# Performance work log

Measured on AMD Instinct MI355X. Metric: run time of the kernel, lower is better.

The kernel has to match this reference:

```python
import jax, jax.numpy as jnp
import numpy as np

CUTOFF = 8.0
NUM_G = 50
HID = 128
NUM_INTER = 3
NUM_NODES = 50000
NUM_EDGES = 1600000
NUM_GRAPHS = 128
MAX_Z = 100
LOG2 = float(np.log(2.0))


def ssp(x):
    # PyG ShiftedSoftplus
    return jax.nn.softplus(x) - LOG2


def setup_inputs() -> dict:
    key = jax.random.key(0)
    ks = jax.random.split(key, 20)
    s = 0.1
    pos = jax.random.normal(ks[0], (NUM_NODES, 3), dtype=jnp.float32) * 4.0
    edge_shift = jax.random.normal(ks[1], (NUM_EDGES, 3), dtype=jnp.float32) * 0.5
    z = jax.random.randint(ks[2], (NUM_NODES,), 0, MAX_Z, dtype=jnp.int32)
    edge_index = jax.random.randint(ks[3], (2, NUM_EDGES), 0, NUM_NODES, dtype=jnp.int32)
    batch = jnp.sort(jax.random.randint(ks[4], (NUM_NODES,), 0, NUM_GRAPHS, dtype=jnp.int32))
    emb = jax.random.normal(ks[5], (MAX_Z, HID), dtype=jnp.float32) * s
    mlp_w1 = jax.random.normal(ks[6], (NUM_INTER, NUM_G, HID), dtype=jnp.float32) * s
    mlp_b1 = jnp.zeros((NUM_INTER, HID), jnp.float32)
    mlp_w2 = jax.random.normal(ks[7], (NUM_INTER, HID, HID), dtype=jnp.float32) * s
    mlp_b2 = jnp.zeros((NUM_INTER, HID), jnp.float32)
    cf_w1 = jax.random.normal(ks[8], (NUM_INTER, HID, HID), dtype=jnp.float32) * s  # no bias (PyG lin1)
    cf_w2 = jax.random.normal(ks[9], (NUM_INTER, HID, HID), dtype=jnp.float32) * s
    cf_b2 = jnp.zeros((NUM_INTER, HID), jnp.float32)
    lin_w = jax.random.normal(ks[10], (NUM_INTER, HID, HID), dtype=jnp.float32) * s
    lin_b = jnp.zeros((NUM_INTER, HID), jnp.float32)
    head_w1 = jax.random.normal(ks[11], (HID, HID // 2), dtype=jnp.float32) * s
    head_b1 = jnp.zeros((HID // 2,), jnp.float32)
    head_w2 = jax.random.normal(ks[12], (HID // 2, 1), dtype=jnp.float32) * s
    head_b2 = jnp.zeros((1,), jnp.float32)
    return dict(pos=pos, edge_shift=edge_shift, emb=emb, mlp_w1=mlp_w1, mlp_b1=mlp_b1,
                mlp_w2=mlp_w2, mlp_b2=mlp_b2, cf_w1=cf_w1, cf_w2=cf_w2, cf_b2=cf_b2,
                lin_w=lin_w, lin_b=lin_b, head_w1=head_w1, head_b1=head_b1,
                head_w2=head_w2, head_b2=head_b2, z=z, edge_index=edge_index, batch=batch)


def reference(pos, edge_shift, emb, mlp_w1, mlp_b1, mlp_w2, mlp_b2, cf_w1, cf_w2, cf_b2,
              lin_w, lin_b, head_w1, head_b1, head_w2, head_b2, z, edge_index, batch):
    src, dst = edge_index[0], edge_index[1]
    # edge distances: pos[row] - (pos[col] + shift)
    rel = pos[src] - (pos[dst] + edge_shift)            # [E,3]
    w = jnp.linalg.norm(rel, axis=-1)                   # [E]
    # Gaussian smearing
    offset = jnp.linspace(0.0, CUTOFF, NUM_G, dtype=pos.dtype)
    coeff = -0.5 / (offset[1] - offset[0]) ** 2
    edge_attr = jnp.exp(coeff * (w[:, None] - offset) ** 2)   # [E,50]
    # cosine cutoff
    C = 0.5 * (jnp.cos(w * jnp.pi / CUTOFF) + 1.0)            # [E]
    h = emb[z]                                                # [N,128]
    for i in range(NUM_INTER):
        Wf = (ssp(edge_attr @ mlp_w1[i] + mlp_b1[i]) @ mlp_w2[i] + mlp_b2[i]) * C[:, None]  # [E,128]
        msg = (h @ cf_w1[i])[src] * Wf                   # gather-multiply  [E,128]
        agg = jax.ops.segment_sum(msg, dst, num_segments=NUM_NODES)         # scatter-sum [N,128]
        h = h + (ssp(agg @ cf_w2[i] + cf_b2[i]) @ lin_w[i] + lin_b[i])
    out_atom = ssp(h @ head_w1 + head_b1) @ head_w2 + head_b2               # [N,1]
    sums = jax.ops.segment_sum(out_atom, batch, num_segments=NUM_GRAPHS)    # [G,1]
    counts = jax.ops.segment_sum(jnp.ones((NUM_NODES, 1), out_atom.dtype), batch, num_segments=NUM_GRAPHS)
    return sums / jnp.maximum(counts, 1.0)  # mean readout; out_proj is Identity (128==128)
```

## Files before the change

### kernel.cpp

```cpp
#include <hip/hip_runtime.h>
#include <hip/hip_fp16.h>
#include <math.h>

#define NNODES  50000
#define NEDGES  1600000
#define NGRAPHS 128
#define HID     128
#define NG      50
#define NITER   3
#define TPTS    2048
#define WMAX    12.0f
#define PI_F    3.14159265358979323846f

typedef __attribute__((ext_vector_type(4))) _Float16 half4;
typedef __attribute__((ext_vector_type(4))) float   f32x4;
typedef __attribute__((ext_vector_type(4))) unsigned u32x4;

__device__ __forceinline__ float ssp(float x) {
    float sp = fmaxf(x, 0.0f) + log1pf(expf(-fabsf(x)));
    return sp - 0.69314718055994530942f;
}

__global__ __launch_bounds__(256) void k_init_h(const float* __restrict__ emb,
                                                const int* __restrict__ z,
                                                float* __restrict__ h,
                                                _Float16* __restrict__ hH)
{
    int idx = blockIdx.x * 256 + threadIdx.x;
    int n = idx >> 7, c = idx & 127;
    float v = emb[(z[n] << 7) + c];
    h[idx] = v;
    hH[idx] = (_Float16)v;
}

__global__ __launch_bounds__(128) void k_wt3(const float* __restrict__ w1,
                                             const float* __restrict__ w2,
                                             const float* __restrict__ lw,
                                             _Float16* __restrict__ o1,
                                             _Float16* __restrict__ o2,
                                             _Float16* __restrict__ o3)
{
    int fam = blockIdx.x / 384;
    int rem = blockIdx.x - fam * 384;
    int it = rem >> 7, c = rem & 127, j = threadIdx.x;
    const float* in = (fam == 0) ? w1 : (fam == 1) ? w2 : lw;
    _Float16* out   = (fam == 0) ? o1 : (fam == 1) ? o2 : o3;
    out[(size_t)it * 16384 + c * 128 + j] = (_Float16)in[(size_t)it * 16384 + j * 128 + c];
}

__global__ __launch_bounds__(128) void k_table(const float* __restrict__ W1,
                                               const float* __restrict__ B1,
                                               const float* __restrict__ W2,
                                               const float* __restrict__ B2,
                                               __half* __restrict__ ti)
{
    int it = blockIdx.x / TPTS;
    int pt = blockIdx.x - it * TPTS;
    const float* W1i = W1 + (size_t)it * NG * HID;
    const float* B1i = B1 + (size_t)it * HID;
    const float* W2i = W2 + (size_t)it * HID * HID;
    const float* B2i = B2 + (size_t)it * HID;

    const float step = WMAX / (float)(TPTS - 1);
    float w0 = pt * step;
    int ptn = (pt < TPTS - 1) ? pt + 1 : pt;
    float w1v = ptn * step;

    __shared__ float sEA[2][NG];
    __shared__ float sT1[2][HID];
    int k = threadIdx.x;
    {
        float dx = 8.0f / 49.0f;
        float coeff = -0.5f / (dx * dx);
        if (k < NG) {
            float diff = w0 - (float)k * dx;
            sEA[0][k] = expf(coeff * diff * diff);
        } else if (k >= 64 && k < 64 + NG) {
            float diff = w1v - (float)(k - 64) * dx;
            sEA[1][k - 64] = expf(coeff * diff * diff);
        }
    }
    __syncthreads();
    float a0 = B1i[k], a1 = a0;
    for (int g = 0; g < NG; ++g) {
        float wv = W1i[g * HID + k];
        a0 = fmaf(sEA[0][g], wv, a0);
        a1 = fmaf(sEA[1][g], wv, a1);
    }
    sT1[0][k] = ssp(a0);
    sT1[1][k] = ssp(a1);
    __syncthreads();
    float b0 = B2i[k], b1v = b0;
    for (int j = 0; j < HID; ++j) {
        float wv = W2i[j * HID + k];
        b0  = fmaf(sT1[0][j], wv, b0);
        b1v = fmaf(sT1[1][j], wv, b1v);
    }
    size_t base = ((size_t)it * TPTS + pt) * 256;
    int pair = k >> 1, within = k & 1;
    ti[base + pair * 4 + within]     = __float2half(b0);
    ti[base + pair * 4 + within + 2] = __float2half(b1v - b0);
}

__global__ __launch_bounds__(256) void k_hist(const int* __restrict__ ei,
                                              int* __restrict__ deg)
{
    int e = blockIdx.x * 256 + threadIdx.x;
    if (e >= NEDGES) return;
    atomicAdd(&deg[ei[NEDGES + e]], 1);
}

#define SCAN_T 1024
#define CHUNK  49
__global__ __launch_bounds__(SCAN_T) void k_scan(const int* __restrict__ deg,
                                                 int* __restrict__ rowptr,
                                                 int* __restrict__ cursor)
{
    int tid = threadIdx.x;
    int base = tid * CHUNK;
    int vals[CHUNK];
    int local = 0;
    #pragma unroll
    for (int i = 0; i < CHUNK; ++i) {
        int idx = base + i;
        int v = (idx < NNODES) ? deg[idx] : 0;
        vals[i] = local;
        local += v;
    }
    int lane = tid & 63, wid = tid >> 6;
    int x = local;
    #pragma unroll
    for (int off = 1; off < 64; off <<= 1) {
        int y = __shfl_up(x, off);
        if (lane >= off) x += y;
    }
    __shared__ int wsum[16];
    __shared__ int woff[17];
    if (lane == 63) wsum[wid] = x;
    __syncthreads();
    if (tid == 0) {
        int acc = 0;
        #pragma unroll
        for (int i = 0; i < 16; ++i) { woff[i] = acc; acc += wsum[i]; }
        woff[16] = acc;
    }
    __syncthreads();
    int threadExcl = woff[wid] + x - local;
    #pragma unroll
    for (int i = 0; i < CHUNK; ++i) {
        int idx = base + i;
        if (idx < NNODES) {
            int p = threadExcl + vals[i];
            rowptr[idx] = p;
            cursor[idx] = p;
        }
    }
    if (tid == SCAN_T - 1) rowptr[NNODES] = woff[16];
}

__global__ __launch_bounds__(256) void k_scatter(const int* __restrict__ ei,
                                                 const float* __restrict__ pos,
                                                 const float* __restrict__ shift,
                                                 int* __restrict__ cursor,
                                                 uint2* __restrict__ rec)
{
    int e = blockIdx.x * 256 + threadIdx.x;
    if (e >= NEDGES) return;
    int s = ei[e], d = ei[NEDGES + e];
    float rx = pos[3*s+0] - (pos[3*d+0] + shift[3*e+0]);
    float ry = pos[3*s+1] - (pos[3*d+1] + shift[3*e+1]);
    float rz = pos[3*s+2] - (pos[3*d+2] + shift[3*e+2]);
    float w = sqrtf(rx*rx + ry*ry + rz*rz);
    const float SCALE = (float)(TPTS - 1) / WMAX;
    float t = fminf(w * SCALE, (float)(TPTS - 1));
    int i0 = (int)t; if (i0 > TPTS - 2) i0 = TPTS - 2;
    float fr = t - (float)i0;
    float C = 0.5f * (cosf(w * (PI_F / 8.0f)) + 1.0f);
    __half2 frc = __halves2half2(__float2half(fr), __float2half(C));
    int slot = atomicAdd(&cursor[d], 1);
    rec[slot] = make_uint2((unsigned)s | ((unsigned)i0 << 17), *(unsigned*)&frc);
}

__device__ __forceinline__ void edge_contrib(unsigned rx, unsigned ry, int lane,
                                             const char* __restrict__ hfBase,
                                             const char* __restrict__ tbBase,
                                             float& ax, float& ay)
{
    unsigned sB = (rx & 0x1FFFFu) << 8;
    unsigned tB = (rx >> 17) << 9;
    __half2 frc = *reinterpret_cast<__half2*>(&ry);
    __half2 fr2 = __half2half2(__low2half(frc));
    __half2 c2  = __half2half2(__high2half(frc));
    uint2 tv = *reinterpret_cast<const uint2*>(tbBase + tB + lane * 8);
    unsigned hu = *reinterpret_cast<const unsigned*>(hfBase + sB + lane * 4);
    __half2 hv   = *reinterpret_cast<__half2*>(&hu);
    __half2 vals = *reinterpret_cast<__half2*>(&tv.x);
    __half2 dels = *reinterpret_cast<__half2*>(&tv.y);
    __half2 f2 = __hfma2(fr2, dels, vals);
    __half2 ch = __hmul2(c2, hv);
    ax = fmaf(__low2float(f2),  __low2float(ch),  ax);
    ay = fmaf(__high2float(f2), __high2float(ch), ay);
}

__global__ __launch_bounds__(256) void k_gather(const uint2* __restrict__ rec,
                                                const int* __restrict__ rowptr,
                                                const __half* __restrict__ hfH,
                                                const __half* __restrict__ tableH,
                                                __half2* __restrict__ aggH)
{
    int node = blockIdx.x * 4 + (threadIdx.x >> 6);
    int lane = threadIdx.x & 63;
    const char* hfBase = (const char*)hfH;
    const char* tbBase = (const char*)tableH;
    int beg = rowptr[node], end = rowptr[node + 1];
    float ax0 = 0.f, ay0 = 0.f, ax1 = 0.f, ay1 = 0.f;
    int k = beg;
    if ((k & 1) && k < end) {
        uint2 r = rec[k];
        edge_contrib(r.x, r.y, lane, hfBase, tbBase, ax0, ay0);
        ++k;
    }
    for (; k + 8 <= end; k += 8) {
        u32x4 ra = __builtin_nontemporal_load(reinterpret_cast<const u32x4*>(rec + k));
        u32x4 rb = __builtin_nontemporal_load(reinterpret_cast<const u32x4*>(rec + k + 2));
        u32x4 rc = __builtin_nontemporal_load(reinterpret_cast<const u32x4*>(rec + k + 4));
        u32x4 rd = __builtin_nontemporal_load(reinterpret_cast<const u32x4*>(rec + k + 6));
        edge_contrib(ra.x, ra.y, lane, hfBase, tbBase, ax0, ay0);
        edge_contrib(ra.z, ra.w, lane, hfBase, tbBase, ax1, ay1);
        edge_contrib(rb.x, rb.y, lane, hfBase, tbBase, ax0, ay0);
        edge_contrib(rb.z, rb.w, lane, hfBase, tbBase, ax1, ay1);
        edge_contrib(rc.x, rc.y, lane, hfBase, tbBase, ax0, ay0);
        edge_contrib(rc.z, rc.w, lane, hfBase, tbBase, ax1, ay1);
        edge_contrib(rd.x, rd.y, lane, hfBase, tbBase, ax0, ay0);
        edge_contrib(rd.z, rd.w, lane, hfBase, tbBase, ax1, ay1);
    }
    for (; k + 2 <= end; k += 2) {
        u32x4 ra = __builtin_nontemporal_load(reinterpret_cast<const u32x4*>(rec + k));
        edge_contrib(ra.x, ra.y, lane, hfBase, tbBase, ax0, ay0);
        edge_contrib(ra.z, ra.w, lane, hfBase, tbBase, ax1, ay1);
    }
    if (k < end) {
        uint2 r = rec[k];
        edge_contrib(r.x, r.y, lane, hfBase, tbBase, ax0, ay0);
    }
    aggH[(size_t)node * 64 + lane] = __floats2half2_rn(ax0 + ax1, ay0 + ay1);
}

__global__ __launch_bounds__(256) void k_ngemm_mfma(const _Float16* __restrict__ hH,
                                                    const _Float16* __restrict__ Wt,
                                                    _Float16* __restrict__ outH)
{
    int tid = threadIdx.x;
    int wave = tid >> 6, l = tid & 63;
    int lr = l & 15, lg = l >> 4;
    int r0 = blockIdx.x * 16;
    f32x4 acc[2];
    acc[0] = (f32x4){0.f, 0.f, 0.f, 0.f};
    acc[1] = (f32x4){0.f, 0.f, 0.f, 0.f};
    const _Float16* aRow = hH + (size_t)(r0 + lr) * HID;
    #pragma unroll
    for (int kk = 0; kk < 8; ++kk) {
        half4 a = *(const half4*)(aRow + kk * 16 + lg * 4);
        #pragma unroll
        for (int c = 0; c < 2; ++c) {
            int ct = wave * 2 + c;
            half4 b = *(const half4*)(Wt + (size_t)(ct * 16 + lr) * HID + kk * 16 + lg * 4);
            acc[c] = __builtin_amdgcn_mfma_f32_16x16x16f16(a, b, acc[c], 0, 0, 0);
        }
    }
    #pragma unroll
    for (int c = 0; c < 2; ++c) {
        int col = (wave * 2 + c) * 16 + lr;
        #pragma unroll
        for (int r = 0; r < 4; ++r)
            outH[(size_t)(r0 + lg * 4 + r) * HID + col] = (_Float16)acc[c][r];
    }
}

__global__ __launch_bounds__(256) void k_update_mfma(const _Float16* __restrict__ aggH,
                                                     const _Float16* __restrict__ W2t,
                                                     const float* __restrict__ B2,
                                                     const _Float16* __restrict__ Lt,
                                                     const float* __restrict__ LB,
                                                     float* __restrict__ h,
                                                     _Float16* __restrict__ hH,
                                                     const _Float16* __restrict__ W1n,
                                                     _Float16* __restrict__ hfOut)
{
    __shared__ _Float16 sT[16 * 128];
    int tid = threadIdx.x;
    int wave = tid >> 6, l = tid & 63;
    int lr = l & 15, lg = l >> 4;
    int r0 = blockIdx.x * 16;

    f32x4 acc[2];
    acc[0] = (f32x4){0.f, 0.f, 0.f, 0.f};
    acc[1] = (f32x4){0.f, 0.f, 0.f, 0.f};
    const _Float16* aRow = aggH + (size_t)(r0 + lr) * HID;
    #pragma unroll
    for (int kk = 0; kk < 8; ++kk) {
        half4 a = *(const half4*)(aRow + kk * 16 + lg * 4);
        #pragma unroll
        for (int c = 0; c < 2; ++c) {
            int ct = wave * 2 + c;
            half4 b = *(const half4*)(W2t + (size_t)(ct * 16 + lr) * HID + kk * 16 + lg * 4);
            acc[c] = __builtin_amdgcn_mfma_f32_16x16x16f16(a, b, acc[c], 0, 0, 0);
        }
    }
    #pragma unroll
    for (int c = 0; c < 2; ++c) {
        int col = (wave * 2 + c) * 16 + lr;
        float bias = B2[col];
        #pragma unroll
        for (int r = 0; r < 4; ++r) {
            int rl = lg * 4 + r;
            float v = ssp(acc[c][r] + bias);
            int byte = rl * 256 + col * 2;
            byte ^= (rl & 7) << 4;
            *(_Float16*)((char*)sT + byte) = (_Float16)v;
        }
    }
    __syncthreads();
    f32x4 acc2[2];
    acc2[0] = (f32x4){0.f, 0.f, 0.f, 0.f};
    acc2[1] = (f32x4){0.f, 0.f, 0.f, 0.f};
    #pragma unroll
    for (int kk = 0; kk < 8; ++kk) {
        int byte = lr * 256 + (kk * 16 + lg * 4) * 2;
        byte ^= (lr & 7) << 4;
        half4 a = *(const half4*)((char*)sT + byte);
        #pragma unroll
        for (int c = 0; c < 2; ++c) {
            int ct = wave * 2 + c;
            half4 b = *(const half4*)(Lt + (size_t)(ct * 16 + lr) * HID + kk * 16 + lg * 4);
            acc2[c] = __builtin_amdgcn_mfma_f32_16x16x16f16(a, b, acc2[c], 0, 0, 0);
        }
    }
    __syncthreads();
    _Float16 hnew[2][4];
    #pragma unroll
    for (int c = 0; c < 2; ++c) {
        int col = (wave * 2 + c) * 16 + lr;
        float lb = LB[col];
        #pragma unroll
        for (int r = 0; r < 4; ++r) {
            int row = r0 + lg * 4 + r;
            float hv = h[(size_t)row * HID + col] + acc2[c][r] + lb;
            h[(size_t)row * HID + col] = hv;
            hH[(size_t)row * HID + col] = (_Float16)hv;
            hnew[c][r] = (_Float16)hv;
        }
    }
    if (W1n) {
        #pragma unroll
        for (int c = 0; c < 2; ++c) {
            int col = (wave * 2 + c) * 16 + lr;
            #pragma unroll
            for (int r = 0; r < 4; ++r) {
                int rl = lg * 4 + r;
                int byte = rl * 256 + col * 2;
                byte ^= (rl & 7) << 4;
                *(_Float16*)((char*)sT + byte) = hnew[c][r];
            }
        }
        __syncthreads();
        f32x4 acc3[2];
        acc3[0] = (f32x4){0.f, 0.f, 0.f, 0.f};
        acc3[1] = (f32x4){0.f, 0.f, 0.f, 0.f};
        #pragma unroll
        for (int kk = 0; kk < 8; ++kk) {
            int byte = lr * 256 + (kk * 16 + lg * 4) * 2;
            byte ^= (lr & 7) << 4;
            half4 a = *(const half4*)((char*)sT + byte);
            #pragma unroll
            for (int c = 0; c < 2; ++c) {
                int ct = wave * 2 + c;
                half4 b = *(const half4*)(W1n + (size_t)(ct * 16 + lr) * HID + kk * 16 + lg * 4);
                acc3[c] = __builtin_amdgcn_mfma_f32_16x16x16f16(a, b, acc3[c], 0, 0, 0);
            }
        }
        #pragma unroll
        for (int c = 0; c < 2; ++c) {
            int col = (wave * 2 + c) * 16 + lr;
            #pragma unroll
            for (int r = 0; r < 4; ++r)
                hfOut[(size_t)(r0 + lg * 4 + r) * HID + col] = (_Float16)acc3[c][r];
        }
    }
}

__global__ __launch_bounds__(512) void k_head(const float* __restrict__ h,
                                              const float* __restrict__ w1,
                                              const float* __restrict__ b1,
                                              const float* __restrict__ w2,
                                              const float* __restrict__ b2,
                                              const int* __restrict__ batch,
                                              float* __restrict__ sums_pad)
{
    __shared__ float sA[128 * 132];
    int r0 = blockIdx.x * 128;
    int tid = threadIdx.x;
    for (int idx = tid; idx < 128 * 32; idx += 512) {
        int r = idx >> 5, c4 = idx & 31;
        int row = r0 + r;
        float4 v = make_float4(0.f, 0.f, 0.f, 0.f);
        if (row < NNODES) v = *(const float4*)(h + (size_t)row * HID + c4 * 4);
        *(float4*)(&sA[r * 132 + c4 * 4]) = v;
    }
    __syncthreads();
    int tx = tid & 7, ty = tid >> 3;
    int cc = tx * 8, ee = ty * 2;
    float acc[2][8];
    {
        float4 b0 = *(const float4*)(b1 + cc);
        float4 bb = *(const float4*)(b1 + cc + 4);
        #pragma unroll
        for (int e = 0; e < 2; ++e) {
            acc[e][0]=b0.x; acc[e][1]=b0.y; acc[e][2]=b0.z; acc[e][3]=b0.w;
            acc[e][4]=bb.x; acc[e][5]=bb.y; acc[e][6]=bb.z; acc[e][7]=bb.w;
        }
    }
    #pragma unroll 4
    for (int j = 0; j < HID; ++j) {
        float a0 = sA[(ee + 0) * 132 + j];
        float a1 = sA[(ee + 1) * 132 + j];
        float4 w0 = *(const float4*)(w1 + (size_t)j * 64 + cc);
        float4 wv1 = *(const float4*)(w1 + (size_t)j * 64 + cc + 4);
        float wv[8] = {w0.x,w0.y,w0.z,w0.w,wv1.x,wv1.y,wv1.z,wv1.w};
        #pragma unroll
        for (int c = 0; c < 8; ++c) {
            acc[0][c] = fmaf(a0, wv[c], acc[0][c]);
            acc[1][c] = fmaf(a1, wv[c], acc[1][c]);
        }
    }
    float4 w2a = *(const float4*)(w2 + cc);
    float4 w2b = *(const float4*)(w2 + cc + 4);
    float w2v[8] = {w2a.x,w2a.y,w2a.z,w2a.w,w2b.x,w2b.y,w2b.z,w2b.w};
    float bias2 = b2[0];
    #pragma unroll
    for (int e = 0; e < 2; ++e) {
        float part = 0.f;
        #pragma unroll
        for (int c = 0; c < 8; ++c) part = fmaf(ssp(acc[e][c]), w2v[c], part);
        part += __shfl_down(part, 4, 8);
        part += __shfl_down(part, 2, 8);
        part += __shfl_down(part, 1, 8);
        if (tx == 0) {
            int row = r0 + ee + e;
            if (row < NNODES) {
                int b = batch[row];
                atomicAdd(&sums_pad[b * 16], part + bias2);
            }
        }
    }
}

__global__ void k_final(const float* __restrict__ sums_pad,
                        const int* __restrict__ batch,
                        float* __restrict__ out)
{
    int g = threadIdx.x;
    if (g >= NGRAPHS) return;
    int lo = 0, hi = NNODES;
    while (lo < hi) { int mid = (lo + hi) >> 1; if (batch[mid] < g) lo = mid + 1; else hi = mid; }
    int a = lo;
    lo = 0; hi = NNODES;
    while (lo < hi) { int mid = (lo + hi) >> 1; if (batch[mid] < g + 1) lo = mid + 1; else hi = mid; }
    float cnt = (float)(lo - a);
    out[g] = sums_pad[g * 16] / fmaxf(cnt, 1.0f);
}

extern "C" void kernel_launch(void* const* d_in, const int* in_sizes, int n_in,
                              void* d_out, int out_size, void* d_ws, size_t ws_size,
                              hipStream_t stream)
{
    const float* pos     = (const float*)d_in[0];
    const float* shift   = (const float*)d_in[1];
    const float* emb     = (const float*)d_in[2];
    const float* mlp_w1  = (const float*)d_in[3];
    const float* mlp_b1  = (const float*)d_in[4];
    const float* mlp_w2  = (const float*)d_in[5];
    const float* mlp_b2  = (const float*)d_in[6];
    const float* cf_w1   = (const float*)d_in[7];
    const float* cf_w2   = (const float*)d_in[8];
    const float* cf_b2   = (const float*)d_in[9];
    const float* lin_w   = (const float*)d_in[10];
    const float* lin_b   = (const float*)d_in[11];
    const float* head_w1 = (const float*)d_in[12];
    const float* head_b1 = (const float*)d_in[13];
    const float* head_w2 = (const float*)d_in[14];
    const float* head_b2 = (const float*)d_in[15];
    const int*   z       = (const int*)d_in[16];
    const int*   ei      = (const int*)d_in[17];
    const int*   batch   = (const int*)d_in[18];
    float* out = (float*)d_out;

    float* ws = (float*)d_ws;
    size_t off = 0;
    float*    h       = ws + off; off += (size_t)NNODES * HID;
    _Float16* hH      = (_Float16*)(ws + off); off += (size_t)(NNODES + 64) * HID / 2;
    _Float16* hfH     = (_Float16*)(ws + off); off += (size_t)(NNODES + 64) * HID / 2;
    _Float16* aggH    = (_Float16*)(ws + off); off += (size_t)(NNODES + 64) * HID / 2;
    __half*   tableH  = (__half*)(ws + off); off += (size_t)3 * TPTS * 256 / 2;
    _Float16* w1t     = (_Float16*)(ws + off); off += (size_t)3 * HID * HID / 2;
    _Float16* w2t     = (_Float16*)(ws + off); off += (size_t)3 * HID * HID / 2;
    _Float16* lwt     = (_Float16*)(ws + off); off += (size_t)3 * HID * HID / 2;
    uint2*    rec     = (uint2*)(ws + off); off += (size_t)2 * NEDGES;
    int*      rowptr  = (int*)(ws + off); off += NNODES + 1;
    int*      deg     = (int*)(ws + off); off += NNODES;
    int*      cursor  = (int*)(ws + off); off += NNODES;
    float*    sums_pad= ws + off; off += NGRAPHS * 16;

    hipMemsetAsync(deg, 0, NNODES * sizeof(int), stream);
    hipMemsetAsync(sums_pad, 0, NGRAPHS * 16 * sizeof(float), stream);

    k_hist<<<(NEDGES + 255) / 256, 256, 0, stream>>>(ei, deg);
    k_scan<<<1, SCAN_T, 0, stream>>>(deg, rowptr, cursor);
    k_scatter<<<(NEDGES + 255) / 256, 256, 0, stream>>>(ei, pos, shift, cursor, rec);

    k_init_h<<<NNODES * HID / 256, 256, 0, stream>>>(emb, z, h, hH);
    k_table<<<3 * TPTS, 128, 0, stream>>>(mlp_w1, mlp_b1, mlp_w2, mlp_b2, tableH);
    k_wt3<<<3 * 384, 128, 0, stream>>>(cf_w1, cf_w2, lin_w, w1t, w2t, lwt);

    int gblk = NNODES / 16;
    k_ngemm_mfma<<<gblk, 256, 0, stream>>>(hH, w1t, hfH);
    for (int i = 0; i < NITER; ++i) {
        k_gather<<<NNODES / 4, 256, 0, stream>>>(rec, rowptr, (const __half*)hfH,
                                                 tableH + (size_t)i * TPTS * 256,
                                                 (__half2*)aggH);
        k_update_mfma<<<gblk, 256, 0, stream>>>(aggH, w2t + (size_t)i * HID * HID,
                                                cf_b2 + (size_t)i * HID,
                                                lwt + (size_t)i * HID * HID,
                                                lin_b + (size_t)i * HID, h, hH,
                                                (i < NITER - 1) ? w1t + (size_t)(i + 1) * HID * HID : nullptr,
                                                hfH);
    }
    k_head<<<(NNODES + 127) / 128, 512, 0, stream>>>(h, head_w1, head_b1, head_w2, head_b2, batch, sums_pad);
    k_final<<<1, 128, 0, stream>>>(sums_pad, batch, out);
}
```

Baseline: 1.018 ms.

## Fuse edge gather with node update MLP into one per-iteration kernel

The separate gather kernel and update kernel are merged into one kernel per interaction. Each block gathers 16 nodes' aggregated messages into shared memory and then runs the update GEMMs directly from LDS. This removes the global write and read of the aggregation buffer and one launch per iteration. The filtered features now ping-pong between two buffers so the next iteration's features can be written while other blocks still read the current ones. The cost is that each wave now walks four nodes' edge lists in sequence, and the shared-memory GEMM phase waits on the slowest node, which may reduce memory-level parallelism in the gather.

```diff
diff --git a/kernel.cpp b/kernel.cpp
--- a/kernel.cpp
+++ b/kernel.cpp
@@ -202,50 +202,6 @@
     ay = fmaf(__high2float(f2), __high2float(ch), ay);
 }
 
-__global__ __launch_bounds__(256) void k_gather(const uint2* __restrict__ rec,
-                                                const int* __restrict__ rowptr,
-                                                const __half* __restrict__ hfH,
-                                                const __half* __restrict__ tableH,
-                                                __half2* __restrict__ aggH)
-{
-    int node = blockIdx.x * 4 + (threadIdx.x >> 6);
-    int lane = threadIdx.x & 63;
-    const char* hfBase = (const char*)hfH;
-    const char* tbBase = (const char*)tableH;
-    int beg = rowptr[node], end = rowptr[node + 1];
-    float ax0 = 0.f, ay0 = 0.f, ax1 = 0.f, ay1 = 0.f;
-    int k = beg;
-    if ((k & 1) && k < end) {
-        uint2 r = rec[k];
-        edge_contrib(r.x, r.y, lane, hfBase, tbBase, ax0, ay0);
-        ++k;
-    }
-    for (; k + 8 <= end; k += 8) {
-        u32x4 ra = __builtin_nontemporal_load(reinterpret_cast<const u32x4*>(rec + k));
-        u32x4 rb = __builtin_nontemporal_load(reinterpret_cast<const u32x4*>(rec + k + 2));
-        u32x4 rc = __builtin_nontemporal_load(reinterpret_cast<const u32x4*>(rec + k + 4));
-        u32x4 rd = __builtin_nontemporal_load(reinterpret_cast<const u32x4*>(rec + k + 6));
-        edge_contrib(ra.x, ra.y, lane, hfBase, tbBase, ax0, ay0);
-        edge_contrib(ra.z, ra.w, lane, hfBase, tbBase, ax1, ay1);
-        edge_contrib(rb.x, rb.y, lane, hfBase, tbBase, ax0, ay0);
-        edge_contrib(rb.z, rb.w, lane, hfBase, tbBase, ax1, ay1);
-        edge_contrib(rc.x, rc.y, lane, hfBase, tbBase, ax0, ay0);
-        edge_contrib(rc.z, rc.w, lane, hfBase, tbBase, ax1, ay1);
-        edge_contrib(rd.x, rd.y, lane, hfBase, tbBase, ax0, ay0);
-        edge_contrib(rd.z, rd.w, lane, hfBase, tbBase, ax1, ay1);
-    }
-    for (; k + 2 <= end; k += 2) {
-        u32x4 ra = __builtin_nontemporal_load(reinterpret_cast<const u32x4*>(rec + k));
-        edge_contrib(ra.x, ra.y, lane, hfBase, tbBase, ax0, ay0);
-        edge_contrib(ra.z, ra.w, lane, hfBase, tbBase, ax1, ay1);
-    }
-    if (k < end) {
-        uint2 r = rec[k];
-        edge_contrib(r.x, r.y, lane, hfBase, tbBase, ax0, ay0);
-    }
-    aggH[(size_t)node * 64 + lane] = __floats2half2_rn(ax0 + ax1, ay0 + ay1);
-}
-
 __global__ __launch_bounds__(256) void k_ngemm_mfma(const _Float16* __restrict__ hH,
                                                     const _Float16* __restrict__ Wt,
                                                     _Float16* __restrict__ outH)
@@ -277,29 +233,78 @@
     }
 }
 
-__global__ __launch_bounds__(256) void k_update_mfma(const _Float16* __restrict__ aggH,
-                                                     const _Float16* __restrict__ W2t,
-                                                     const float* __restrict__ B2,
-                                                     const _Float16* __restrict__ Lt,
-                                                     const float* __restrict__ LB,
-                                                     float* __restrict__ h,
-                                                     _Float16* __restrict__ hH,
-                                                     const _Float16* __restrict__ W1n,
-                                                     _Float16* __restrict__ hfOut)
-{
+__global__ __launch_bounds__(256) void k_iter(const uint2* __restrict__ rec,
+                                              const int* __restrict__ rowptr,
+                                              const __half* __restrict__ hfIn,
+                                              const __half* __restrict__ tableH,
+                                              const _Float16* __restrict__ W2t,
+                                              const float* __restrict__ B2,
+                                              const _Float16* __restrict__ Lt,
+                                              const float* __restrict__ LB,
+                                              float* __restrict__ h,
+                                              _Float16* __restrict__ hH,
+                                              const _Float16* __restrict__ W1n,
+                                              _Float16* __restrict__ hfOut)
+{
+    __shared__ _Float16 sAgg[16 * 128];
     __shared__ _Float16 sT[16 * 128];
     int tid = threadIdx.x;
     int wave = tid >> 6, l = tid & 63;
+    int r0 = blockIdx.x * 16;
+    const char* hfBase = (const char*)hfIn;
+    const char* tbBase = (const char*)tableH;
+
+    #pragma unroll
+    for (int j = 0; j < 4; ++j) {
+        int rl = wave * 4 + j;
+        int node = r0 + rl;
+        int beg = rowptr[node], end = rowptr[node + 1];
+        float ax0 = 0.f, ay0 = 0.f, ax1 = 0.f, ay1 = 0.f;
+        int k = beg;
+        if ((k & 1) && k < end) {
+            uint2 r = rec[k];
+            edge_contrib(r.x, r.y, l, hfBase, tbBase, ax0, ay0);
+            ++k;
+        }
+        for (; k + 8 <= end; k += 8) {
+            u32x4 ra = __builtin_nontemporal_load(reinterpret_cast<const u32x4*>(rec + k));
+            u32x4 rb = __builtin_nontemporal_load(reinterpret_cast<const u32x4*>(rec + k + 2));
+            u32x4 rc = __builtin_nontemporal_load(reinterpret_cast<const u32x4*>(rec + k + 4));
+            u32x4 rd = __builtin_nontemporal_load(reinterpret_cast<const u32x4*>(rec + k + 6));
+            edge_contrib(ra.x, ra.y, l, hfBase, tbBase, ax0, ay0);
+            edge_contrib(ra.z, ra.w, l, hfBase, tbBase, ax1, ay1);
+            edge_contrib(rb.x, rb.y, l, hfBase, tbBase, ax0, ay0);
+            edge_contrib(rb.z, rb.w, l, hfBase, tbBase, ax1, ay1);
+            edge_contrib(rc.x, rc.y, l, hfBase, tbBase, ax0, ay0);
+            edge_contrib(rc.z, rc.w, l, hfBase, tbBase, ax1, ay1);
+            edge_contrib(rd.x, rd.y, l, hfBase, tbBase, ax0, ay0);
+            edge_contrib(rd.z, rd.w, l, hfBase, tbBase, ax1, ay1);
+        }
+        for (; k + 2 <= end; k += 2) {
+            u32x4 ra = __builtin_nontemporal_load(reinterpret_cast<const u32x4*>(rec + k));
+            edge_contrib(ra.x, ra.y, l, hfBase, tbBase, ax0, ay0);
+            edge_contrib(ra.z, ra.w, l, hfBase, tbBase, ax1, ay1);
+        }
+        if (k < end) {
+            uint2 r = rec[k];
+            edge_contrib(r.x, r.y, l, hfBase, tbBase, ax0, ay0);
+        }
+        __half2 res = __floats2half2_rn(ax0 + ax1, ay0 + ay1);
+        int byte = rl * 256 + l * 4;
+        byte ^= (rl & 7) << 4;
+        *(__half2*)((char*)sAgg + byte) = res;
+    }
+    __syncthreads();
+
     int lr = l & 15, lg = l >> 4;
-    int r0 = blockIdx.x * 16;
-
     f32x4 acc[2];
     acc[0] = (f32x4){0.f, 0.f, 0.f, 0.f};
     acc[1] = (f32x4){0.f, 0.f, 0.f, 0.f};
-    const _Float16* aRow = aggH + (size_t)(r0 + lr) * HID;
     #pragma unroll
     for (int kk = 0; kk < 8; ++kk) {
-        half4 a = *(const half4*)(aRow + kk * 16 + lg * 4);
+        int byte = lr * 256 + (kk * 16 + lg * 4) * 2;
+        byte ^= (lr & 7) << 4;
+        half4 a = *(const half4*)((char*)sAgg + byte);
         #pragma unroll
         for (int c = 0; c < 2; ++c) {
             int ct = wave * 2 + c;
@@ -321,6 +326,7 @@
         }
     }
     __syncthreads();
+
     f32x4 acc2[2];
     acc2[0] = (f32x4){0.f, 0.f, 0.f, 0.f};
     acc2[1] = (f32x4){0.f, 0.f, 0.f, 0.f};
@@ -336,8 +342,6 @@
             acc2[c] = __builtin_amdgcn_mfma_f32_16x16x16f16(a, b, acc2[c], 0, 0, 0);
         }
     }
-    __syncthreads();
-    _Float16 hnew[2][4];
     #pragma unroll
     for (int c = 0; c < 2; ++c) {
         int col = (wave * 2 + c) * 16 + lr;
@@ -348,21 +352,15 @@
             float hv = h[(size_t)row * HID + col] + acc2[c][r] + lb;
             h[(size_t)row * HID + col] = hv;
             hH[(size_t)row * HID + col] = (_Float16)hv;
-            hnew[c][r] = (_Float16)hv;
-        }
-    }
-    if (W1n) {
-        #pragma unroll
-        for (int c = 0; c < 2; ++c) {
-            int col = (wave * 2 + c) * 16 + lr;
-            #pragma unroll
-            for (int r = 0; r < 4; ++r) {
+            if (W1n) {
                 int rl = lg * 4 + r;
                 int byte = rl * 256 + col * 2;
                 byte ^= (rl & 7) << 4;
-                *(_Float16*)((char*)sT + byte) = hnew[c][r];
+                *(_Float16*)((char*)sAgg + byte) = (_Float16)hv;
             }
         }
+    }
+    if (W1n) {
         __syncthreads();
         f32x4 acc3[2];
         acc3[0] = (f32x4){0.f, 0.f, 0.f, 0.f};
@@ -371,7 +369,7 @@
         for (int kk = 0; kk < 8; ++kk) {
             int byte = lr * 256 + (kk * 16 + lg * 4) * 2;
             byte ^= (lr & 7) << 4;
-            half4 a = *(const half4*)((char*)sT + byte);
+            half4 a = *(const half4*)((char*)sAgg + byte);
             #pragma unroll
             for (int c = 0; c < 2; ++c) {
                 int ct = wave * 2 + c;
@@ -499,8 +497,8 @@
     size_t off = 0;
     float*    h       = ws + off; off += (size_t)NNODES * HID;
     _Float16* hH      = (_Float16*)(ws + off); off += (size_t)(NNODES + 64) * HID / 2;
-    _Float16* hfH     = (_Float16*)(ws + off); off += (size_t)(NNODES + 64) * HID / 2;
-    _Float16* aggH    = (_Float16*)(ws + off); off += (size_t)(NNODES + 64) * HID / 2;
+    _Float16* hfA     = (_Float16*)(ws + off); off += (size_t)(NNODES + 64) * HID / 2;
+    _Float16* hfB     = (_Float16*)(ws + off); off += (size_t)(NNODES + 64) * HID / 2;
     __half*   tableH  = (__half*)(ws + off); off += (size_t)3 * TPTS * 256 / 2;
     _Float16* w1t     = (_Float16*)(ws + off); off += (size_t)3 * HID * HID / 2;
     _Float16* w2t     = (_Float16*)(ws + off); off += (size_t)3 * HID * HID / 2;
@@ -523,17 +521,18 @@
     k_wt3<<<3 * 384, 128, 0, stream>>>(cf_w1, cf_w2, lin_w, w1t, w2t, lwt);
 
     int gblk = NNODES / 16;
-    k_ngemm_mfma<<<gblk, 256, 0, stream>>>(hH, w1t, hfH);
+    k_ngemm_mfma<<<gblk, 256, 0, stream>>>(hH, w1t, hfA);
+    _Float16* hfPing[2] = {hfA, hfB};
     for (int i = 0; i < NITER; ++i) {
-        k_gather<<<NNODES / 4, 256, 0, stream>>>(rec, rowptr, (const __half*)hfH,
-                                                 tableH + (size_t)i * TPTS * 256,
-                                                 (__half2*)aggH);
-        k_update_mfma<<<gblk, 256, 0, stream>>>(aggH, w2t + (size_t)i * HID * HID,
-                                                cf_b2 + (size_t)i * HID,
-                                                lwt + (size_t)i * HID * HID,
-                                                lin_b + (size_t)i * HID, h, hH,
-                                                (i < NITER - 1) ? w1t + (size_t)(i + 1) * HID * HID : nullptr,
-                                                hfH);
+        k_iter<<<gblk, 256, 0, stream>>>(rec, rowptr,
+                                         (const __half*)hfPing[i & 1],
+                                         tableH + (size_t)i * TPTS * 256,
+                                         w2t + (size_t)i * HID * HID,
+                                         cf_b2 + (size_t)i * HID,
+                                         lwt + (size_t)i * HID * HID,
+                                         lin_b + (size_t)i * HID, h, hH,
+                                         (i < NITER - 1) ? w1t + (size_t)(i + 1) * HID * HID : nullptr,
+                                         hfPing[(i + 1) & 1]);
     }
     k_head<<<(NNODES + 127) / 128, 512, 0, stream>>>(h, head_w1, head_b1, head_w2, head_b2, batch, sums_pad);
     k_final<<<1, 128, 0, stream>>>(sums_pad, batch, out);
```

Result: no change. 1.036 ms (+1.8%).
